# Kernel tuning notes

Measured on AMD Instinct MI355X. Metric: run time of the kernel, lower is better.

Reference implementation:

```python
import jax, jax.numpy as jnp
import numpy as np

X_DIM = 40
N_BATCH = 65536


def _circ_conv1d(x, W, b, pad):
    # x: [N, C_in, L], W: [C_out, C_in, K] (torch layout), circular padding
    if pad > 0:
        x = jnp.pad(x, ((0, 0), (0, 0), (pad, pad)), mode='wrap')
    y = jax.lax.conv_general_dilated(x, W, window_strides=(1,), padding='VALID',
                                     dimension_numbers=('NCH', 'OIH', 'NCH'))
    return y + b[None, :, None]


def setup_inputs() -> dict:
    key = jax.random.key(0)
    ks = jax.random.split(key, 9)
    u = jax.random.normal(ks[0], (N_BATCH, X_DIM), dtype=jnp.float32)
    coeff = jax.random.normal(ks[1], (18,), dtype=jnp.float32) * 0.1
    # Conv1d params, torch layout [out_ch, in_ch, kernel], kaiming-ish scale
    W1 = jax.random.normal(ks[2], (72, 1, 5), dtype=jnp.float32) * (1.0 / np.sqrt(1 * 5))
    b1 = jax.random.normal(ks[3], (72,), dtype=jnp.float32) * 0.05
    W2 = jax.random.normal(ks[4], (37, 48, 5), dtype=jnp.float32) * (1.0 / np.sqrt(48 * 5))
    b2 = jax.random.normal(ks[5], (37,), dtype=jnp.float32) * 0.05
    W3 = jax.random.normal(ks[6], (1, 37, 1), dtype=jnp.float32) * (1.0 / np.sqrt(37))
    b3 = jax.random.normal(ks[7], (1,), dtype=jnp.float32) * 0.05
    t = jnp.zeros((1,), dtype=jnp.float32)  # unused by the module, kept for signature fidelity
    return {"t": t, "u": u, "coeff": coeff, "W1": W1, "b1": b1,
            "W2": W2, "b2": b2, "W3": W3, "b3": b3}


def reference(t, u, coeff, W1, b1, W2, b2, W3, b3):
    # circular neighbor gathers: index_select with (i+k)%D == roll by -k
    u_m2 = jnp.roll(u, 2, axis=-1)
    u_m1 = jnp.roll(u, 1, axis=-1)
    u_p1 = jnp.roll(u, -1, axis=-1)
    u_p2 = jnp.roll(u, -2, axis=-1)
    feats = jnp.stack([
        jnp.ones_like(u),
        u_m2, u_m1, u, u_p1, u_p2,
        u_m2 ** 2, u_m1 ** 2, u ** 2, u_p1 ** 2, u_p2 ** 2,
        u_m2 * u_m1, u_m1 * u, u * u_p1, u_p1 * u_p2,
        u_m2 * u, u_m1 * u_p1, u * u_p2,
    ], axis=-1)  # [N, D, 18]
    out1 = feats @ coeff  # [N, D]

    x = u[:, None, :]  # [N, 1, D]
    h = jax.nn.relu(_circ_conv1d(x, W1, b1, 2))  # [N, 72, D]
    h = jnp.concatenate([h[:, :24], h[:, 24:48] * h[:, 48:]], axis=1)  # [N, 48, D]
    h = jax.nn.relu(_circ_conv1d(h, W2, b2, 2))  # [N, 37, D]
    out2 = _circ_conv1d(h, W3, b3, 0)[:, 0, :]  # [N, D]
    return out1 + out2
```

## Files before the change

kernel.cpp:

```cpp
#include <hip/hip_runtime.h>
#include <hip/hip_bf16.h>

typedef short s16x8 __attribute__((ext_vector_type(8)));
typedef short s16x4 __attribute__((ext_vector_type(4)));
typedef float f32x4 __attribute__((ext_vector_type(4)));

#define TB 8
#define NBG 16
#define HALO 46
#define GSTRIDE 2216
#define USTRIDE 50
#define NT 3
#define GT_SHORTS (TB * GSTRIDE)

__device__ __forceinline__ unsigned short f2bf(float f) {
    unsigned int u = __float_as_uint(f);
    u += 0x7fff + ((u >> 16) & 1);
    return (unsigned short)(u >> 16);
}

__device__ __forceinline__ unsigned int pk_bf16(float lo, float hi) {
    float2 f; f.x = lo; f.y = hi;
    __hip_bfloat162 h = __float22bfloat162_rn(f);
    union { __hip_bfloat162 b; unsigned int u; } c;
    c.b = h;
    return c.u;
}

__device__ __forceinline__ float sload(const float* p) {
    return __uint_as_float(__builtin_amdgcn_readfirstlane(__float_as_uint(*p)));
}

__global__ __launch_bounds__(256, 2) void lorenz96_fused(
    const float* __restrict__ u,
    const float* __restrict__ coeff,
    const float* __restrict__ W1,
    const float* __restrict__ b1,
    const float* __restrict__ W2,
    const float* __restrict__ b2,
    const float* __restrict__ W3,
    const float* __restrict__ b3,
    float* __restrict__ out)
{
    __shared__ __align__(16) unsigned short gtile[2][GT_SHORTS];
    __shared__ __align__(16) float u_sbuf[2][TB * USTRIDE];

    unsigned short* B_lds = &gtile[0][0];

    const int t    = threadIdx.x;
    const int lane = t & 63;
    const int wave = t >> 6;
    const int quad = lane >> 4;
    const int l15  = lane & 15;

    const int b0_block = blockIdx.x * (TB * NBG);

    for (int g = t; g < NT * 8 * 64; g += 256) {
        int lg = g & 63;
        int ks = (g >> 6) & 7;
        int nt = g >> 9;
        int o  = nt * 16 + (lg & 15);
        int kb = ks * 32 + (lg >> 4) * 8;
        s16x8 pack = {0, 0, 0, 0, 0, 0, 0, 0};
        #pragma unroll
        for (int j = 0; j < 8; ++j) {
            int k = kb + j;
            if (o < 37) {
                if (k < 240) {
                    int c = k % 48, tap = k / 48;
                    pack[j] = (short)f2bf(W2[o * 240 + c * 5 + tap]);
                } else if (k == 240) {
                    pack[j] = (short)f2bf(b2[o]);
                }
            }
        }
        *(s16x8*)&B_lds[g * 8] = pack;
    }

    s16x8 aW1[5];
    {
        int chs[5];
        chs[0] = l15; chs[1] = 16 + l15; chs[2] = 32 + l15;
        chs[3] = (l15 >= 8) ? 40 + l15 : -1;
        chs[4] = 56 + l15;
        #pragma unroll
        for (int mt = 0; mt < 5; ++mt) {
            s16x8 a = {0, 0, 0, 0, 0, 0, 0, 0};
            int ch = chs[mt];
            if (quad == 0 && ch >= 0) {
                #pragma unroll
                for (int j = 0; j < 5; ++j) a[j] = (short)f2bf(W1[ch * 5 + j]);
                a[5] = (short)f2bf(b1[ch]);
            }
            aW1[mt] = a;
        }
    }

    float w3v[NT][4];
    #pragma unroll
    for (int nt = 0; nt < NT; ++nt)
        #pragma unroll
        for (int r = 0; r < 4; ++r) {
            int o = nt * 16 + quad * 4 + r;
            w3v[nt][r] = (o < 37) ? W3[o] : 0.f;
        }
    const float b3v = sload(b3);
    float cf[18];
    #pragma unroll
    for (int i = 0; i < 18; ++i) cf[i] = sload(&coeff[i]);

    s16x8 aW2[NT][8];
    float pv_q = 0.f, pv_4 = 0.f;
    float st_v0 = 0.f, st_v1 = 0.f;

    auto prestage_u = [&](int grp) {
        for (int idx = t; idx < TB * USTRIDE; idx += 256) {
            int b = idx / USTRIDE, k = idx - b * USTRIDE;
            int gi = k + 36; gi -= (gi >= 40) ? 40 : 0; gi -= (gi >= 40) ? 40 : 0;
            u_sbuf[grp & 1][idx] = u[(size_t)(b0_block + grp * TB + b) * 40 + gi];
        }
    };

    auto prestage_issue = [&](int grp) {
        {
            int idx = t;
            int b = idx / USTRIDE, k = idx - b * USTRIDE;
            int gi = k + 36; gi -= (gi >= 40) ? 40 : 0; gi -= (gi >= 40) ? 40 : 0;
            st_v0 = u[(size_t)(b0_block + grp * TB + b) * 40 + gi];
        }
        if (t + 256 < TB * USTRIDE) {
            int idx = t + 256;
            int b = idx / USTRIDE, k = idx - b * USTRIDE;
            int gi = k + 36; gi -= (gi >= 40) ? 40 : 0; gi -= (gi >= 40) ? 40 : 0;
            st_v1 = u[(size_t)(b0_block + grp * TB + b) * 40 + gi];
        }
    };

    auto prestage_commit = [&](int grp) {
        u_sbuf[grp & 1][t] = st_v0;
        if (t + 256 < TB * USTRIDE) u_sbuf[grp & 1][t + 256] = st_v1;
    };

    auto poly1 = [&](const float* u_s, int m) -> float {
        int p = m >> 3, b = m & 7;
        const float* us = &u_s[b * USTRIDE + p];
        float um2 = us[2], um1 = us[3], u0 = us[4], up1 = us[5], up2 = us[6];
        return cf[0] + cf[1]*um2 + cf[2]*um1 + cf[3]*u0 + cf[4]*up1 + cf[5]*up2
             + cf[6]*um2*um2 + cf[7]*um1*um1 + cf[8]*u0*u0 + cf[9]*up1*up1 + cf[10]*up2*up2
             + cf[11]*um2*um1 + cf[12]*um1*u0 + cf[13]*u0*up1 + cf[14]*up1*up2
             + cf[15]*um2*u0 + cf[16]*um1*up1 + cf[17]*u0*up2;
    };

    auto phase2 = [&](int gi) {
        const float* u_s = u_sbuf[gi & 1];
        unsigned short* gt = &gtile[gi & 1][0];
        #pragma unroll
        for (int i = 0; i < 6; ++i) {
            const int ct = wave + 4 * i;
            if (ct > 22) continue;
            const int col = ct * 16 + l15;
            const int b = col & 7, h = col >> 3;
            s16x8 bU = {0, 0, 0, 0, 0, 0, 0, 0};
            if (quad == 0) {
                const float* us = &u_s[b * USTRIDE + h];
                union { s16x8 v; unsigned int w[4]; } bu;
                bu.w[0] = pk_bf16(us[0], us[1]);
                bu.w[1] = pk_bf16(us[2], us[3]);
                bu.w[2] = pk_bf16(us[4], 1.0f);
                bu.w[3] = 0;
                bU = bu.v;
            }
            f32x4 a0 = {0.f,0.f,0.f,0.f}, a1 = a0, a2 = a0, a3 = a0, a4 = a0;
            a0 = __builtin_amdgcn_mfma_f32_16x16x32_bf16(aW1[0], bU, a0, 0, 0, 0);
            a1 = __builtin_amdgcn_mfma_f32_16x16x32_bf16(aW1[1], bU, a1, 0, 0, 0);
            a2 = __builtin_amdgcn_mfma_f32_16x16x32_bf16(aW1[2], bU, a2, 0, 0, 0);
            a3 = __builtin_amdgcn_mfma_f32_16x16x32_bf16(aW1[3], bU, a3, 0, 0, 0);
            a4 = __builtin_amdgcn_mfma_f32_16x16x32_bf16(aW1[4], bU, a4, 0, 0, 0);
            float v0[4], v1[4], v2[4];
            #pragma unroll
            for (int r = 0; r < 4; ++r) {
                v0[r] = fmaxf(a0[r], 0.f);
                v1[r] = fmaxf(a1[r], 0.f);
                if (quad >= 2) v1[r] *= fmaxf(a3[r], 0.f);
                v2[r] = fmaxf(a2[r], 0.f) * fmaxf(a4[r], 0.f);
            }
            union { s16x4 v; unsigned int w[2]; } w0, w1, w2;
            w0.w[0] = pk_bf16(v0[0], v0[1]); w0.w[1] = pk_bf16(v0[2], v0[3]);
            w1.w[0] = pk_bf16(v1[0], v1[1]); w1.w[1] = pk_bf16(v1[2], v1[3]);
            w2.w[0] = pk_bf16(v2[0], v2[1]); w2.w[1] = pk_bf16(v2[2], v2[3]);
            unsigned short* gp = &gt[b * GSTRIDE + h * 48 + quad * 4];
            *(s16x4*)(gp)      = w0.v;
            *(s16x4*)(gp + 16) = w1.v;
            *(s16x4*)(gp + 32) = w2.v;
        }
    };

    auto p3_tile = [&](int i, const unsigned short* gt, int b0) {
        const int mt = wave + 4 * i;
        const int m  = mt * 16 + l15;
        const int p  = m >> 3, b = m & 7;
        const unsigned short* gbase = &gt[b * GSTRIDE + p * 48 + quad * 8];
        s16x8 bg[8];
        #pragma unroll
        for (int ks = 0; ks < 8; ++ks) bg[ks] = *(const s16x8*)(gbase + ks * 32);
        {
            s16x8 b7 = bg[7];
            if (quad == 2) b7[0] = (short)0x3F80;
            bg[7] = b7;
        }
        f32x4 c0 = {0.f,0.f,0.f,0.f}, c1 = c0, c2 = c0;
        #pragma unroll
        for (int ks = 0; ks < 8; ++ks) {
            c0 = __builtin_amdgcn_mfma_f32_16x16x32_bf16(aW2[0][ks], bg[ks], c0, 0, 0, 0);
            c1 = __builtin_amdgcn_mfma_f32_16x16x32_bf16(aW2[1][ks], bg[ks], c1, 0, 0, 0);
            c2 = __builtin_amdgcn_mfma_f32_16x16x32_bf16(aW2[2][ks], bg[ks], c2, 0, 0, 0);
        }
        float s = 0.f;
        #pragma unroll
        for (int r = 0; r < 4; ++r) {
            s += fmaxf(c0[r], 0.f) * w3v[0][r];
            s += fmaxf(c1[r], 0.f) * w3v[1][r];
            s += fmaxf(c2[r], 0.f) * w3v[2][r];
        }
        s += __shfl_xor(s, 16, 64);
        s += __shfl_xor(s, 32, 64);
        const float pv = (i < 4) ? pv_q : pv_4;
        const bool  st = (i < 4) ? (quad == i) : (quad == 0);
        if (st) {
            out[(size_t)(b0 + (l15 & 7)) * 40 + 2 * mt + (l15 >> 3)] = s + b3v + pv;
        }
    };

    prestage_u(0);
    __syncthreads();

    #pragma unroll
    for (int nt = 0; nt < NT; ++nt)
        #pragma unroll
        for (int ks = 0; ks < 8; ++ks)
            aW2[nt][ks] = *(const s16x8*)&B_lds[((nt * 8 + ks) * 64 + lane) * 8];

    {
        const float* u_s = u_sbuf[0];
        pv_q = poly1(u_s, (wave + 4 * quad) * 16 + l15);
        pv_4 = poly1(u_s, (wave + 16) * 16 + l15);
    }
    prestage_u(1);
    __syncthreads();

    phase2(0);
    __syncthreads();

    for (int g = 0; g < NBG; ++g) {
        const int b0 = b0_block + g * TB;
        const unsigned short* gt = &gtile[g & 1][0];

        if (g + 2 < NBG) prestage_issue(g + 2);

        float tq = 0.f, t4 = 0.f;
        if (g + 1 < NBG) {
            const float* u_s = u_sbuf[(g + 1) & 1];
            tq = poly1(u_s, (wave + 4 * quad) * 16 + l15);
            t4 = poly1(u_s, (wave + 16) * 16 + l15);
        }

        #pragma unroll
        for (int i = 0; i < 5; ++i) p3_tile(i, gt, b0);

        if (g + 1 < NBG) {
            phase2(g + 1);
            if (g + 2 < NBG) prestage_commit(g + 2);
            pv_q = tq; pv_4 = t4;
            __syncthreads();
        }
    }
}

extern "C" void kernel_launch(void* const* d_in, const int* in_sizes, int n_in,
                              void* d_out, int out_size, void* d_ws, size_t ws_size,
                              hipStream_t stream) {
    const float* u     = (const float*)d_in[1];
    const float* coeff = (const float*)d_in[2];
    const float* W1    = (const float*)d_in[3];
    const float* b1    = (const float*)d_in[4];
    const float* W2    = (const float*)d_in[5];
    const float* b2    = (const float*)d_in[6];
    const float* W3    = (const float*)d_in[7];
    const float* b3    = (const float*)d_in[8];
    float* out = (float*)d_out;

    const int n_batch = in_sizes[1] / 40;
    const int grid = n_batch / (TB * NBG);
    lorenz96_fused<<<grid, 256, 0, stream>>>(u, coeff, W1, b1, W2, b2, W3, b3, out);
}
```

Before: 180.1 us.

## Use six waves per block and move third W2 tile to LDS

Grows each block from 4 to 6 waves and remaps the phase-2 column tiles and phase-3 output tiles across the 6 waves. The third W2 output tile, which holds only 5 live rows, and the W3 weights now live in LDS instead of registers, and the B operand is loaded in two halves. Together these cut register pressure so more waves fit per SIMD (launch bounds 384,3). The cost is extra LDS reads inside the MFMA loop and uneven work across waves.

```diff
diff --git a/kernel.cpp b/kernel.cpp
--- a/kernel.cpp
+++ b/kernel.cpp
@@ -7,6 +7,8 @@
 
 #define TB 8
 #define NBG 16
+#define WAVES 6
+#define NTHREADS (WAVES * 64)
 #define HALO 46
 #define GSTRIDE 2216
 #define USTRIDE 50
@@ -31,7 +33,7 @@
     return __uint_as_float(__builtin_amdgcn_readfirstlane(__float_as_uint(*p)));
 }
 
-__global__ __launch_bounds__(256, 2) void lorenz96_fused(
+__global__ __launch_bounds__(NTHREADS, 3) void lorenz96_fused(
     const float* __restrict__ u,
     const float* __restrict__ coeff,
     const float* __restrict__ W1,
@@ -44,6 +46,8 @@
 {
     __shared__ __align__(16) unsigned short gtile[2][GT_SHORTS];
     __shared__ __align__(16) float u_sbuf[2][TB * USTRIDE];
+    __shared__ __align__(16) unsigned short W2sz[8 * 4 * 5 * 8 + 8];
+    __shared__ __align__(16) float W3l[48];
 
     unsigned short* B_lds = &gtile[0][0];
 
@@ -55,7 +59,7 @@
 
     const int b0_block = blockIdx.x * (TB * NBG);
 
-    for (int g = t; g < NT * 8 * 64; g += 256) {
+    for (int g = t; g < NT * 8 * 64; g += NTHREADS) {
         int lg = g & 63;
         int ks = (g >> 6) & 7;
         int nt = g >> 9;
@@ -74,8 +78,14 @@
                 }
             }
         }
-        *(s16x8*)&B_lds[g * 8] = pack;
+        if (nt < 2) {
+            *(s16x8*)&B_lds[g * 8] = pack;
+        } else if ((lg & 15) < 5) {
+            *(s16x8*)&W2sz[((ks * 4 + (lg >> 4)) * 5 + (lg & 15)) * 8] = pack;
+        }
     }
+    if (t < 8)  W2sz[1280 + t] = 0;
+    if (t < 48) W3l[t] = (t < 37) ? W3[t] : 0.f;
 
     s16x8 aW1[5];
     {
@@ -96,25 +106,23 @@
         }
     }
 
-    float w3v[NT][4];
-    #pragma unroll
-    for (int nt = 0; nt < NT; ++nt)
-        #pragma unroll
-        for (int r = 0; r < 4; ++r) {
-            int o = nt * 16 + quad * 4 + r;
-            w3v[nt][r] = (o < 37) ? W3[o] : 0.f;
-        }
     const float b3v = sload(b3);
     float cf[18];
     #pragma unroll
     for (int i = 0; i < 18; ++i) cf[i] = sload(&coeff[i]);
 
-    s16x8 aW2[NT][8];
-    float pv_q = 0.f, pv_4 = 0.f;
+    s16x8 aW2[2][8];
+    float pv_q = 0.f;
+    const int mtqc = min(wave + WAVES * quad, 19);
+    const int a2idx  = (l15 < 5) ? (quad * 5 + l15) * 8 : 1280;
+    const int a2step = (l15 < 5) ? 160 : 0;
     float st_v0 = 0.f, st_v1 = 0.f;
 
+    const int c_start = (wave < 2) ? wave * 3 : wave * 4 - 2;
+    const int c_cnt   = (wave < 2) ? 3 : ((wave == 5) ? 5 : 4);
+
     auto prestage_u = [&](int grp) {
-        for (int idx = t; idx < TB * USTRIDE; idx += 256) {
+        for (int idx = t; idx < TB * USTRIDE; idx += NTHREADS) {
             int b = idx / USTRIDE, k = idx - b * USTRIDE;
             int gi = k + 36; gi -= (gi >= 40) ? 40 : 0; gi -= (gi >= 40) ? 40 : 0;
             u_sbuf[grp & 1][idx] = u[(size_t)(b0_block + grp * TB + b) * 40 + gi];
@@ -128,8 +136,8 @@
             int gi = k + 36; gi -= (gi >= 40) ? 40 : 0; gi -= (gi >= 40) ? 40 : 0;
             st_v0 = u[(size_t)(b0_block + grp * TB + b) * 40 + gi];
         }
-        if (t + 256 < TB * USTRIDE) {
-            int idx = t + 256;
+        if (t + NTHREADS < TB * USTRIDE) {
+            int idx = t + NTHREADS;
             int b = idx / USTRIDE, k = idx - b * USTRIDE;
             int gi = k + 36; gi -= (gi >= 40) ? 40 : 0; gi -= (gi >= 40) ? 40 : 0;
             st_v1 = u[(size_t)(b0_block + grp * TB + b) * 40 + gi];
@@ -138,7 +146,7 @@
 
     auto prestage_commit = [&](int grp) {
         u_sbuf[grp & 1][t] = st_v0;
-        if (t + 256 < TB * USTRIDE) u_sbuf[grp & 1][t + 256] = st_v1;
+        if (t + NTHREADS < TB * USTRIDE) u_sbuf[grp & 1][t + NTHREADS] = st_v1;
     };
 
     auto poly1 = [&](const float* u_s, int m) -> float {
@@ -155,9 +163,9 @@
         const float* u_s = u_sbuf[gi & 1];
         unsigned short* gt = &gtile[gi & 1][0];
         #pragma unroll
-        for (int i = 0; i < 6; ++i) {
-            const int ct = wave + 4 * i;
-            if (ct > 22) continue;
+        for (int ii = 0; ii < 5; ++ii) {
+            if (ii >= c_cnt) continue;
+            const int ct = c_start + ii;
             const int col = ct * 16 + l15;
             const int b = col & 7, h = col >> 3;
             s16x8 bU = {0, 0, 0, 0, 0, 0, 0, 0};
@@ -196,38 +204,44 @@
     };
 
     auto p3_tile = [&](int i, const unsigned short* gt, int b0) {
-        const int mt = wave + 4 * i;
+        const int mt = wave + WAVES * i;
         const int m  = mt * 16 + l15;
         const int p  = m >> 3, b = m & 7;
         const unsigned short* gbase = &gt[b * GSTRIDE + p * 48 + quad * 8];
-        s16x8 bg[8];
-        #pragma unroll
-        for (int ks = 0; ks < 8; ++ks) bg[ks] = *(const s16x8*)(gbase + ks * 32);
-        {
-            s16x8 b7 = bg[7];
-            if (quad == 2) b7[0] = (short)0x3F80;
-            bg[7] = b7;
-        }
         f32x4 c0 = {0.f,0.f,0.f,0.f}, c1 = c0, c2 = c0;
         #pragma unroll
-        for (int ks = 0; ks < 8; ++ks) {
-            c0 = __builtin_amdgcn_mfma_f32_16x16x32_bf16(aW2[0][ks], bg[ks], c0, 0, 0, 0);
-            c1 = __builtin_amdgcn_mfma_f32_16x16x32_bf16(aW2[1][ks], bg[ks], c1, 0, 0, 0);
-            c2 = __builtin_amdgcn_mfma_f32_16x16x32_bf16(aW2[2][ks], bg[ks], c2, 0, 0, 0);
+        for (int half = 0; half < 2; ++half) {
+            s16x8 bg[4];
+            #pragma unroll
+            for (int j = 0; j < 4; ++j) bg[j] = *(const s16x8*)(gbase + (half * 4 + j) * 32);
+            if (half == 1) {
+                s16x8 b7 = bg[3];
+                if (quad == 2) b7[0] = (short)0x3F80;
+                bg[3] = b7;
+            }
+            #pragma unroll
+            for (int j = 0; j < 4; ++j) {
+                const int ks = half * 4 + j;
+                s16x8 a2 = *(const s16x8*)&W2sz[a2idx + ks * a2step];
+                c0 = __builtin_amdgcn_mfma_f32_16x16x32_bf16(aW2[0][ks], bg[j], c0, 0, 0, 0);
+                c1 = __builtin_amdgcn_mfma_f32_16x16x32_bf16(aW2[1][ks], bg[j], c1, 0, 0, 0);
+                c2 = __builtin_amdgcn_mfma_f32_16x16x32_bf16(a2,         bg[j], c2, 0, 0, 0);
+            }
         }
         float s = 0.f;
+        const f32x4 w30 = *(const f32x4*)&W3l[0 * 16 + quad * 4];
+        const f32x4 w31 = *(const f32x4*)&W3l[1 * 16 + quad * 4];
+        const f32x4 w32 = *(const f32x4*)&W3l[2 * 16 + quad * 4];
         #pragma unroll
         for (int r = 0; r < 4; ++r) {
-            s += fmaxf(c0[r], 0.f) * w3v[0][r];
-            s += fmaxf(c1[r], 0.f) * w3v[1][r];
-            s += fmaxf(c2[r], 0.f) * w3v[2][r];
+            s += fmaxf(c0[r], 0.f) * w30[r];
+            s += fmaxf(c1[r], 0.f) * w31[r];
+            s += fmaxf(c2[r], 0.f) * w32[r];
         }
         s += __shfl_xor(s, 16, 64);
         s += __shfl_xor(s, 32, 64);
-        const float pv = (i < 4) ? pv_q : pv_4;
-        const bool  st = (i < 4) ? (quad == i) : (quad == 0);
-        if (st) {
-            out[(size_t)(b0 + (l15 & 7)) * 40 + 2 * mt + (l15 >> 3)] = s + b3v + pv;
+        if (quad == i) {
+            out[(size_t)(b0 + (l15 & 7)) * 40 + 2 * mt + (l15 >> 3)] = s + b3v + pv_q;
         }
     };
 
@@ -235,16 +249,12 @@
     __syncthreads();
 
     #pragma unroll
-    for (int nt = 0; nt < NT; ++nt)
+    for (int nt = 0; nt < 2; ++nt)
         #pragma unroll
         for (int ks = 0; ks < 8; ++ks)
             aW2[nt][ks] = *(const s16x8*)&B_lds[((nt * 8 + ks) * 64 + lane) * 8];
 
-    {
-        const float* u_s = u_sbuf[0];
-        pv_q = poly1(u_s, (wave + 4 * quad) * 16 + l15);
-        pv_4 = poly1(u_s, (wave + 16) * 16 + l15);
-    }
+    pv_q = poly1(u_sbuf[0], mtqc * 16 + l15);
     prestage_u(1);
     __syncthreads();
 
@@ -257,20 +267,20 @@
 
         if (g + 2 < NBG) prestage_issue(g + 2);
 
-        float tq = 0.f, t4 = 0.f;
-        if (g + 1 < NBG) {
-            const float* u_s = u_sbuf[(g + 1) & 1];
-            tq = poly1(u_s, (wave + 4 * quad) * 16 + l15);
-            t4 = poly1(u_s, (wave + 16) * 16 + l15);
-        }
-
-        #pragma unroll
-        for (int i = 0; i < 5; ++i) p3_tile(i, gt, b0);
+        float tq = 0.f;
+        if (g + 1 < NBG)
+            tq = poly1(u_sbuf[(g + 1) & 1], mtqc * 16 + l15);
+
+        #pragma unroll
+        for (int i = 0; i < 4; ++i) {
+            if (wave + WAVES * i >= 20) continue;
+            p3_tile(i, gt, b0);
+        }
 
         if (g + 1 < NBG) {
             phase2(g + 1);
             if (g + 2 < NBG) prestage_commit(g + 2);
-            pv_q = tq; pv_4 = t4;
+            pv_q = tq;
             __syncthreads();
         }
     }
@@ -291,5 +301,5 @@
 
     const int n_batch = in_sizes[1] / 40;
     const int grid = n_batch / (TB * NBG);
-    lorenz96_fused<<<grid, 256, 0, stream>>>(u, coeff, W1, b1, W2, b2, W3, b3, out);
-}
+    lorenz96_fused<<<grid, NTHREADS, 0, stream>>>(u, coeff, W1, b1, W2, b2, W3, b3, out);
+}
```

Measured after the change: 254.2 us. +41.1%, slower.
